# Kernel optimization log

Hardware: AMD Instinct MI355X
Metric: run time of the kernel (lower is better)

## Reference

```python
import jax, jax.numpy as jnp
import numpy as np

B, S, D, H, HD = 2, 1024, 1024, 16, 64
CKV, CQ, R, DFF, L, V = 256, 384, 32, 2816, 4, 32000
EPS = 1.1920929e-07  # torch RMSNorm default eps = finfo(float32).eps


def rmsnorm(x, w):
    return x * jax.lax.rsqrt(jnp.mean(x * x, -1, keepdims=True) + EPS) * w


def rope(x, base=10000.0):
    # x: [B, H, S, d]; GPT-NeoX style rotate-half, matches RoPE._neg_half
    d, s = x.shape[-1], x.shape[2]
    theta = 1.0 / base ** (jnp.arange(0, d, 2, dtype=jnp.float32) / d)
    ang = jnp.arange(s, dtype=jnp.float32)[:, None] * theta[None, :]
    ang = jnp.concatenate([ang, ang], -1)  # [s, d]
    neg = jnp.concatenate([-x[..., d // 2:], x[..., :d // 2]], -1)
    return x * jnp.cos(ang) + neg * jnp.sin(ang)


def forward(tokens, embed, w_kv_down, b_kv_down, w_q_down, b_q_down, w_kv_up, b_kv_up,
            w_q_up, b_q_up, w_o, b_o, kv_norm_w, q_norm_w, norm1_w, norm2_w,
            w_in, b_in, w_out, b_out, norm_f_w, w_head, b_head):
    h = embed[tokens]                                  # [B, S, D]
    causal = jnp.triu(jnp.ones((S, S), bool), 1)       # True above diagonal -> masked
    scale = np.float32(1.0 / np.sqrt(HD + R))
    for i in range(L):
        xn = rmsnorm(h, norm1_w[i])
        ckv = xn @ w_kv_down[i] + b_kv_down[i]         # [B, S, CKV+R]
        c_kv, k_rope = ckv[..., :CKV], ckv[..., CKV:]
        kv = rmsnorm(c_kv, kv_norm_w[i]) @ w_kv_up[i] + b_kv_up[i]
        kv = kv.reshape(B, S, H, 2 * HD).transpose(0, 2, 1, 3)  # [B, H, S, 2*HD]
        k, v = kv[..., :HD], kv[..., HD:]
        qf = rmsnorm(xn @ w_q_down[i] + b_q_down[i], q_norm_w[i]) @ w_q_up[i] + b_q_up[i]
        qf = qf.reshape(B, S, H, HD + R).transpose(0, 2, 1, 3)   # [B, H, S, HD+R]
        q, q_rope = qf[..., :HD], qf[..., HD:]
        k_rope = rope(k_rope[:, None, :, :])           # [B, 1, S, R], shared across heads
        q_rope = rope(q_rope)
        k = jnp.concatenate([k, jnp.broadcast_to(k_rope, (B, H, S, R))], -1)
        q = jnp.concatenate([q, q_rope], -1)
        a = jnp.einsum('bhqd,bhkd->bhqk', q, k) * scale
        a = jax.nn.softmax(jnp.where(causal, -jnp.inf, a), -1)
        attn = jnp.einsum('bhqk,bhkd->bhqd', a, v).transpose(0, 2, 1, 3).reshape(B, S, D)
        h = h + attn @ w_o[i] + b_o[i]
        uv = rmsnorm(h, norm2_w[i]) @ w_in[i] + b_in[i]  # [B, S, 2*DFF]
        h = h + (uv[..., :DFF] * jax.nn.silu(uv[..., DFF:])) @ w_out[i] + b_out[i]
    return rmsnorm(h, norm_f_w) @ w_head + b_head        # [B, S, V]


def setup_inputs() -> dict:
    key = jax.random.key(0)
    it = iter(jax.random.split(key, 24))
    w = lambda shp: jax.random.normal(next(it), shp, jnp.float32) * 0.02
    return dict(
        tokens=jax.random.randint(next(it), (B, S), 0, V),
        embed=w((V, D)),
        w_kv_down=w((L, D, CKV + R)), b_kv_down=w((L, CKV + R)),
        w_q_down=w((L, D, CQ)), b_q_down=w((L, CQ)),
        w_kv_up=w((L, CKV, 2 * HD * H)), b_kv_up=w((L, 2 * HD * H)),
        w_q_up=w((L, CQ, (HD + R) * H)), b_q_up=w((L, (HD + R) * H)),
        w_o=w((L, D, D)), b_o=w((L, D)),
        kv_norm_w=jnp.ones((L, CKV)), q_norm_w=jnp.ones((L, CQ)),
        norm1_w=jnp.ones((L, D)), norm2_w=jnp.ones((L, D)),
        w_in=w((L, D, 2 * DFF)), b_in=w((L, 2 * DFF)),
        w_out=w((L, DFF, D)), b_out=w((L, D)),
        norm_f_w=jnp.ones((D,)),
        w_head=w((D, V)), b_head=w((V,)),
    )


def reference(tokens, embed, w_kv_down, b_kv_down, w_q_down, b_q_down, w_kv_up, b_kv_up,
              w_q_up, b_q_up, w_o, b_o, kv_norm_w, q_norm_w, norm1_w, norm2_w,
              w_in, b_in, w_out, b_out, norm_f_w, w_head, b_head):
    return forward(tokens, embed, w_kv_down, b_kv_down, w_q_down, b_q_down, w_kv_up,
                   b_kv_up, w_q_up, b_q_up, w_o, b_o, kv_norm_w, q_norm_w, norm1_w,
                   norm2_w, w_in, b_in, w_out, b_out, norm_f_w, w_head, b_head)
```

## Files before the change

kernel.cpp:

```cpp
#include <hip/hip_runtime.h>
#include <cstdint>
#include <cstddef>

typedef unsigned short u16;
typedef __attribute__((__ext_vector_type__(8))) __bf16 bf16x8;
typedef __attribute__((__ext_vector_type__(4))) float f32x4;
typedef __attribute__((__ext_vector_type__(8))) unsigned short u16x8;

#define DEVI __device__ __forceinline__

constexpr int Bb = 2, Ss = 1024, Dd = 1024, Hh = 16;
constexpr int Mm = Bb * Ss;
constexpr int QKD = 128;
constexpr float EPSF = 1.1920929e-07f;
constexpr float NEG = -1e30f;
constexpr float QSCALE = 0.10206207261596577f;
constexpr float LOG1E4_16 = 9.210340371976184f / 16.f;

DEVI u16 f2b(float f) {
  union { float f; uint32_t u; } a; a.f = f;
  uint32_t r = a.u + 0x7FFFu + ((a.u >> 16) & 1u);
  return (u16)(r >> 16);
}
DEVI float b2f(u16 h) {
  union { uint32_t u; float f; } a; a.u = ((uint32_t)h) << 16; return a.f;
}

struct WJob { const float* src; u16* dst; int K; int N; int perm; int ntiles; };
struct WJobs { WJob j[7]; };

__global__ __launch_bounds__(256) void k_wcvt_batch(WJobs jobs, int njobs) {
  int t = blockIdx.x;
  int ji = 0;
  while (ji < njobs - 1 && t >= jobs.j[ji].ntiles) { t -= jobs.j[ji].ntiles; ++ji; }
  const float* __restrict__ src = jobs.j[ji].src;
  u16* __restrict__ dst = jobs.j[ji].dst;
  const int K = jobs.j[ji].K, N = jobs.j[ji].N, perm = jobs.j[ji].perm;
  const int ktiles = K >> 6;
  const int bk = (t % ktiles) * 64;
  const int bn = (t / ktiles) * 64;
  __shared__ float ts[64][65];
  const int tid = threadIdx.x;
  {
    int c4 = tid & 15, r = tid >> 4;
    #pragma unroll
    for (int p = 0; p < 4; ++p) {
      int row = r + p * 16;
      int col = bn + c4 * 4;
      float4 v = make_float4(0.f, 0.f, 0.f, 0.f);
      if (col < N) v = *(const float4*)(src + (size_t)(bk + row) * N + col);
      ts[row][c4 * 4 + 0] = v.x; ts[row][c4 * 4 + 1] = v.y;
      ts[row][c4 * 4 + 2] = v.z; ts[row][c4 * 4 + 3] = v.w;
    }
  }
  __syncthreads();
  {
    int k8 = tid & 7, c = tid >> 3;
    #pragma unroll
    for (int p = 0; p < 2; ++p) {
      int cc = c + p * 32;
      int gcol = bn + cc;
      int row = perm ? ((gcol < 2816) ? (gcol * 2) : ((gcol - 2816) * 2 + 1)) : gcol;
      u16x8 o;
      #pragma unroll
      for (int q = 0; q < 8; ++q) o[q] = f2b(ts[k8 * 8 + q][cc]);
      *(u16x8*)(dst + (size_t)row * K + bk + k8 * 8) = o;
    }
  }
}

__global__ void k_embed(const int* __restrict__ tok, const float* __restrict__ emb,
                        float* __restrict__ h) {
  int m = blockIdx.x;
  int t = tok[m];
  const float4* src = (const float4*)(emb + (size_t)t * Dd);
  float4* dst = (float4*)(h + (size_t)m * Dd);
  dst[threadIdx.x] = src[threadIdx.x];
}

__global__ void k_rms(const float* __restrict__ in, int inStride,
                      const float* __restrict__ w, u16* __restrict__ out, int K) {
  int m = blockIdx.x;
  const float* x = in + (size_t)m * inStride;
  float ss = 0.f;
  for (int i = threadIdx.x; i < K; i += 256) { float v = x[i]; ss += v * v; }
  #pragma unroll
  for (int off = 32; off; off >>= 1) ss += __shfl_xor(ss, off);
  __shared__ float red[4];
  if ((threadIdx.x & 63) == 0) red[threadIdx.x >> 6] = ss;
  __syncthreads();
  float r = rsqrtf((red[0] + red[1] + red[2] + red[3]) / (float)K + EPSF);
  for (int i = threadIdx.x; i < K; i += 256)
    out[(size_t)m * K + i] = f2b(x[i] * r * w[i]);
}

__global__ void k_biascat(const float* __restrict__ b1, const float* __restrict__ b2,
                          float* __restrict__ out) {
  int i = blockIdx.x * 256 + threadIdx.x;
  float v = 0.f;
  if (i < 288) v = b1[i];
  else if (i >= 384) v = b2[i - 384];
  out[i] = v;
}

__global__ void k_buildqk(const float* __restrict__ qf, const u16* __restrict__ kv,
                          const float* __restrict__ ckvq, u16* __restrict__ Q,
                          u16* __restrict__ Kb) {
  int s = blockIdx.x, bh = blockIdx.y;
  int b = bh >> 4, h = bh & 15;
  int d = threadIdx.x;
  int m = b * Ss + s;
  int j = d - 64;
  float sn = 0.f, cs = 0.f;
  if (d >= 64 && d < 96) {
    float theta = __expf(-(float)(j & 15) * LOG1E4_16);
    __sincosf((float)s * theta, &sn, &cs);
  }
  const float* qrow = qf + (size_t)m * (Hh * 96) + h * 96;
  float qv = 0.f;
  if (d < 64) qv = qrow[d];
  else if (d < 96) {
    float x = qrow[64 + j], o = qrow[64 + (j ^ 16)];
    qv = x * cs + ((j < 16) ? -o : o) * sn;
  }
  Q[((size_t)bh * Ss + s) * QKD + d] = f2b(qv * QSCALE);
  u16 kvv = 0;
  if (d < 64) kvv = kv[(size_t)m * 2048 + h * 128 + d];
  else if (d < 96) {
    const float* rr = ckvq + (size_t)m * 768 + 256;
    float x = rr[j], o = rr[j ^ 16];
    kvv = f2b(x * cs + ((j < 16) ? -o : o) * sn);
  }
  Kb[((size_t)bh * Ss + s) * QKD + d] = kvv;
}

__global__ void k_buildvt(const u16* __restrict__ kv, u16* __restrict__ Vt) {
  __shared__ u16 t[32][33];
  int bh = blockIdx.x, s0 = blockIdx.y * 32, d0 = blockIdx.z * 32;
  int b = bh >> 4, h = bh & 15;
  int tx = threadIdx.x, ty = threadIdx.y;
  #pragma unroll
  for (int i = ty; i < 32; i += 8) {
    int s = s0 + i, d = d0 + tx;
    t[i][tx] = kv[(size_t)(b * Ss + s) * 2048 + h * 128 + 64 + d];
  }
  __syncthreads();
  #pragma unroll
  for (int i = ty; i < 32; i += 8) {
    int d = d0 + i, s = s0 + tx;
    Vt[((size_t)bh * 64 + d) * Ss + s] = t[tx][i];
  }
}

#define GAS __attribute__((address_space(1)))
#define LAS __attribute__((address_space(3)))
DEVI void gll16(const void* g, void* l) {
  __builtin_amdgcn_global_load_lds((GAS const void*)g, (LAS void*)l, 16, 0, 0);
}
#define VMW(n) asm volatile("s_waitcnt vmcnt(" #n ")" ::: "memory")
#define FENCE asm volatile("" ::: "memory")

__global__ __launch_bounds__(256) void k_flash(
    const u16* __restrict__ Qg, const u16* __restrict__ Kg,
    const u16* __restrict__ Vtg, u16* __restrict__ attn) {
  __shared__ u16 lK[2][64 * 128];
  __shared__ u16 lV[2][64 * 64];
  __shared__ u16 lP[4][16 * 64];
  const int tid = threadIdx.x;
  const int qt = blockIdx.x, bh = blockIdx.y;
  const int b = bh >> 4, h = bh & 15;
  const int lane = tid & 63, w = tid >> 6;
  const int g = lane >> 4, fr = lane & 15;
  const u16* Qh = Qg + (size_t)bh * Ss * QKD;
  const u16* Kh = Kg + (size_t)bh * Ss * QKD;
  const u16* Vh = Vtg + (size_t)bh * 64 * Ss;

  auto stageKV = [&](int buf, int kt) {
    int r = tid >> 4, c = tid & 15;
    #pragma unroll
    for (int gg = 0; gg < 4; ++gg) {
      int row = gg * 16 + r;
      const u16* src = Kh + (size_t)(kt * 64 + row) * QKD + ((c ^ (row & 7)) * 8);
      gll16(src, (u16*)lK[buf] + gg * 2048 + tid * 8);
    }
    int r2 = tid >> 3, c2 = tid & 7;
    #pragma unroll
    for (int gg = 0; gg < 2; ++gg) {
      int d = gg * 32 + r2;
      const u16* src = Vh + (size_t)d * Ss + kt * 64 + ((c2 ^ (d & 7)) * 8);
      gll16(src, (u16*)lV[buf] + gg * 2048 + tid * 8);
    }
  };

  const int q0 = qt * 64;
  bf16x8 af[4];
  const u16* qrow = Qh + (size_t)(q0 + w * 16 + fr) * QKD + g * 8;
  #pragma unroll
  for (int k4 = 0; k4 < 4; ++k4) af[k4] = *(const bf16x8*)(qrow + k4 * 32);

  f32x4 acc_o[4] = {};
  float mrow = NEG, lrow = 0.f;

  stageKV(0, 0);

  for (int kt = 0; kt <= qt; ++kt) {
    const int cur = kt & 1;
    if (kt < qt) { stageKV(cur ^ 1, kt + 1); VMW(6); }
    else { VMW(0); }
    __builtin_amdgcn_s_barrier();
    FENCE;

    f32x4 accs[4] = {};
    #pragma unroll
    for (int j = 0; j < 4; ++j) {
      #pragma unroll
      for (int k4 = 0; k4 < 4; ++k4) {
        int row = j * 16 + fr;
        int ch = (k4 * 4 + g) ^ (row & 7);
        bf16x8 kf = *(const bf16x8*)&lK[cur][row * 128 + ch * 8];
        accs[j] = __builtin_amdgcn_mfma_f32_16x16x32_bf16(kf, af[k4], accs[j], 0, 0, 0);
      }
    }

    float p[16];
    float tmax = NEG;
    #pragma unroll
    for (int j = 0; j < 4; ++j)
      #pragma unroll
      for (int r = 0; r < 4; ++r) {
        float s = accs[j][r];
        int kloc = j * 16 + 4 * g + r;
        bool valid = (kt < qt) || (kloc <= w * 16 + fr);
        s = valid ? s : NEG;
        p[j * 4 + r] = s;
        tmax = fmaxf(tmax, s);
      }
    tmax = fmaxf(tmax, __shfl_xor(tmax, 16));
    tmax = fmaxf(tmax, __shfl_xor(tmax, 32));
    float mnew = fmaxf(mrow, tmax);
    float scale = __expf(mrow - mnew);
    float tsum = 0.f;
    #pragma unroll
    for (int i = 0; i < 16; ++i) { p[i] = __expf(p[i] - mnew); tsum += p[i]; }
    tsum += __shfl_xor(tsum, 16);
    tsum += __shfl_xor(tsum, 32);
    lrow = lrow * scale + tsum;
    mrow = mnew;

    #pragma unroll
    for (int j = 0; j < 4; ++j)
      #pragma unroll
      for (int t = 0; t < 2; ++t) {
        uint32_t u = (uint32_t)f2b(p[j * 4 + 2 * t]) |
                     ((uint32_t)f2b(p[j * 4 + 2 * t + 1]) << 16);
        int kp = 8 * j + 2 * g + t;
        int ch = kp >> 2, wi = kp & 3;
        ((uint32_t*)lP[w])[fr * 32 + ((ch ^ (fr & 7)) << 2) + wi] = u;
      }

    float sc_q[4];
    #pragma unroll
    for (int r = 0; r < 4; ++r) sc_q[r] = __shfl(scale, 4 * g + r);
    #pragma unroll
    for (int j2 = 0; j2 < 4; ++j2)
      #pragma unroll
      for (int r = 0; r < 4; ++r) acc_o[j2][r] *= sc_q[r];

    #pragma unroll
    for (int ksub = 0; ksub < 2; ++ksub) {
      int chp = (4 * ksub + g) ^ (fr & 7);
      bf16x8 pa = *(const bf16x8*)&((const u16*)lP[w])[fr * 64 + chp * 8];
      #pragma unroll
      for (int j2 = 0; j2 < 4; ++j2) {
        int d = j2 * 16 + fr;
        int chv = (ksub * 4 + g) ^ (d & 7);
        bf16x8 vf = *(const bf16x8*)&lV[cur][d * 64 + chv * 8];
        acc_o[j2] = __builtin_amdgcn_mfma_f32_16x16x32_bf16(pa, vf, acc_o[j2], 0, 0, 0);
      }
    }
    FENCE;
    __builtin_amdgcn_s_barrier();
    FENCE;
  }

  float li[4];
  #pragma unroll
  for (int r = 0; r < 4; ++r) li[r] = 1.f / __shfl(lrow, 4 * g + r);
  #pragma unroll
  for (int j2 = 0; j2 < 4; ++j2)
    #pragma unroll
    for (int r = 0; r < 4; ++r) {
      int q = q0 + w * 16 + 4 * g + r;
      int d = j2 * 16 + fr;
      attn[((size_t)(b * Ss) + q) * Dd + h * 64 + d] = f2b(acc_o[j2][r] * li[r]);
    }
}

template <int MODE>
__global__ __launch_bounds__(512, 4) void k_gemm256b(
    const u16* __restrict__ A, const u16* __restrict__ Bt,
    const float* __restrict__ bias, void* __restrict__ Cv,
    int N, int K) {
  __shared__ u16 lA[2][128 * 32];
  __shared__ u16 lB[2][256 * 32];
  const int tid = threadIdx.x;
  const int gx = gridDim.x;
  const int nwg = gx * gridDim.y;
  const int f = blockIdx.y * gx + blockIdx.x;
  const int f2 = (f & 7) * (nwg >> 3) + (f >> 3);
  const int bx = f2 % gx, by = f2 / gx;
  const long m0 = (long)bx * 128, n0 = (long)by * 256;
  const int lane = tid & 63, wid = tid >> 6;
  const int wm = (wid >> 2) * 64, wn = (wid & 3) * 64;
  const int fr = lane & 15, l4 = lane >> 4;
  const int sw = (fr >> 1) & 3;

  const int ra = tid >> 2;
  const int ca = ((tid & 3) ^ ((ra >> 1) & 3)) * 8;
  const u16* a0 = A + (m0 + ra) * (long)K + ca;
  const int rb = tid >> 2;
  const int cb0 = ((tid & 3) ^ ((rb >> 1) & 3)) * 8;
  const int cb1 = ((tid & 3) ^ (((rb + 128) >> 1) & 3)) * 8;
  const u16* b0 = Bt + (n0 + rb) * (long)K + cb0;
  const u16* b1 = Bt + (n0 + rb + 128) * (long)K + cb1;

  f32x4 acc[4][4] = {};
  const int NT = K >> 5;

  gll16(a0, (u16*)lA[0] + tid * 8);
  gll16(b0, (u16*)lB[0] + tid * 8);
  gll16(b1, (u16*)lB[0] + 4096 + tid * 8);

  for (int j = 0; j < NT; ++j) {
    const int cur = j & 1;
    const int kk1 = (j + 1) << 5;
    if (j + 1 < NT) {
      gll16(a0 + kk1, (u16*)lA[cur ^ 1] + tid * 8);
      gll16(b0 + kk1, (u16*)lB[cur ^ 1] + tid * 8);
      gll16(b1 + kk1, (u16*)lB[cur ^ 1] + 4096 + tid * 8);
      VMW(3);
    } else {
      VMW(0);
    }
    __builtin_amdgcn_s_barrier();
    FENCE;
    bf16x8 af[4], bfv[4];
    #pragma unroll
    for (int i = 0; i < 4; ++i)
      af[i] = *(const bf16x8*)&lA[cur][(wm + i * 16 + fr) * 32 + ((l4 ^ sw) * 8)];
    #pragma unroll
    for (int jj = 0; jj < 4; ++jj)
      bfv[jj] = *(const bf16x8*)&lB[cur][(wn + jj * 16 + fr) * 32 + ((l4 ^ sw) * 8)];
    #pragma unroll
    for (int i = 0; i < 4; ++i)
      #pragma unroll
      for (int jj = 0; jj < 4; ++jj)
        acc[i][jj] = __builtin_amdgcn_mfma_f32_16x16x32_bf16(af[i], bfv[jj], acc[i][jj], 0, 0, 0);
    FENCE;
    __builtin_amdgcn_s_barrier();
    FENCE;
  }

  const long r0 = m0 + wm + l4 * 4;
  const long c0 = n0 + wn + fr;
  if (MODE == 0) {
    float* C = (float*)Cv;
    #pragma unroll
    for (int j = 0; j < 4; ++j) {
      long col = c0 + j * 16;
      float bs = bias[col];
      #pragma unroll
      for (int i = 0; i < 4; ++i)
        #pragma unroll
        for (int r = 0; r < 4; ++r)
          C[(r0 + i * 16 + r) * (long)N + col] = acc[i][j][r] + bs;
    }
  } else {
    u16* G = (u16*)Cv;
    #pragma unroll
    for (int j = 0; j < 4; ++j) {
      long col = c0 + j * 16;
      int pcol = (int)((col & 1) ? (col >> 1) + 2816 : (col >> 1));
      float bs = bias[pcol];
      #pragma unroll
      for (int i = 0; i < 4; ++i)
        #pragma unroll
        for (int r = 0; r < 4; ++r) {
          float val = acc[i][j][r] + bs;
          float oth = __shfl_xor(val, 1);
          if (!(col & 1)) {
            float x = oth;
            float gv = val * x * (1.f / (1.f + __expf(-x)));
            G[(r0 + i * 16 + r) * 2816L + (col >> 1)] = f2b(gv);
          }
        }
    }
  }
}

template <int MODE, int BN, bool SWZ>
__global__ __launch_bounds__(256, 4) void k_gemm(
    const u16* __restrict__ A, const u16* __restrict__ Bt,
    const float* __restrict__ bias, void* __restrict__ C,
    int N, int K, long sA, long sB, long sC) {
  __shared__ u16 lA[2][128 * 32];
  __shared__ u16 lB[2][BN * 32];
  const int tid = threadIdx.x;
  const int bz = blockIdx.z;

  int bx, by;
  if (SWZ) {
    int gx = gridDim.x;
    int nwg = gx * gridDim.y;
    int f = blockIdx.y * gx + blockIdx.x;
    int f2 = (f & 7) * (nwg >> 3) + (f >> 3);
    bx = f2 % gx; by = f2 / gx;
  } else {
    bx = blockIdx.x; by = blockIdx.y;
  }
  const long m0 = (long)bx * 128, n0 = (long)by * BN;

  const u16* Az = A + (size_t)bz * sA;
  const u16* Bz = Bt + (size_t)bz * sB;
  const int srow = tid >> 2;
  const int scol = (tid & 3) << 3;
  const u16* a0 = Az + (m0 + srow) * (long)K + scol;
  const u16* b0 = Bz + (n0 + srow) * (long)K + scol;
  const long rstep = 64L * K;

  const int lane = tid & 63, wid = tid >> 6;
  constexpr int WR = (BN == 128) ? 64 : 32;
  constexpr int MI = WR / 16;
  const int wm = (BN == 128) ? (wid >> 1) * 64 : wid * 32;
  const int wn = (BN == 128) ? (wid & 1) * 64 : 0;
  const int fr = lane & 15, kg = (lane >> 4) * 8;

  f32x4 acc[MI][4] = {};
  const int NT = K >> 5;

  gll16(a0, (u16*)lA[0] + tid * 8);
  gll16(a0 + rstep, (u16*)lA[0] + 2048 + tid * 8);
  gll16(b0, (u16*)lB[0] + tid * 8);
  if (BN == 128) gll16(b0 + rstep, (u16*)lB[0] + 2048 + tid * 8);

  for (int j = 0; j < NT; ++j) {
    const int cur = j & 1;
    const int kk1 = (j + 1) << 5;
    if (j + 1 < NT) {
      gll16(a0 + kk1, (u16*)lA[cur ^ 1] + tid * 8);
      gll16(a0 + rstep + kk1, (u16*)lA[cur ^ 1] + 2048 + tid * 8);
      gll16(b0 + kk1, (u16*)lB[cur ^ 1] + tid * 8);
      if (BN == 128) {
        gll16(b0 + rstep + kk1, (u16*)lB[cur ^ 1] + 2048 + tid * 8);
        VMW(4);
      } else {
        VMW(3);
      }
    } else {
      VMW(0);
    }
    __builtin_amdgcn_s_barrier();
    FENCE;
    bf16x8 af[MI], bfr[4];
    #pragma unroll
    for (int i = 0; i < MI; i++) af[i] = *(const bf16x8*)&lA[cur][(wm + i * 16 + fr) * 32 + kg];
    #pragma unroll
    for (int jj = 0; jj < 4; jj++) bfr[jj] = *(const bf16x8*)&lB[cur][(wn + jj * 16 + fr) * 32 + kg];
    #pragma unroll
    for (int i = 0; i < MI; i++)
      #pragma unroll
      for (int jj = 0; jj < 4; jj++)
        acc[i][jj] = __builtin_amdgcn_mfma_f32_16x16x32_bf16(af[i], bfr[jj], acc[i][jj], 0, 0, 0);
    FENCE;
    __builtin_amdgcn_s_barrier();
    FENCE;
  }

  const int rb = wm + ((lane >> 4) << 2);
  const int cb = wn + (lane & 15);
  #pragma unroll
  for (int j = 0; j < 4; j++) {
    long gcol = n0 + cb + j * 16;
    float bs = 0.f;
    if (gcol < N) bs = bias[gcol];
    #pragma unroll
    for (int i = 0; i < MI; i++) {
      #pragma unroll
      for (int r = 0; r < 4; r++) {
        long grow = m0 + rb + i * 16 + r;
        float val = acc[i][j][r];
        if (gcol < N) {
          if (MODE == 0) {
            ((float*)C)[grow * N + gcol] = val + bs;
          } else if (MODE == 1) {
            float* p = (float*)C + grow * N + gcol; *p += val + bs;
          } else {
            ((u16*)C)[grow * N + gcol] = f2b(val + bs);
          }
        }
      }
    }
  }
}

extern "C" void kernel_launch(void* const* d_in, const int* in_sizes, int n_in,
                              void* d_out, int out_size, void* d_ws, size_t ws_size,
                              hipStream_t stream) {
  (void)in_sizes; (void)n_in; (void)out_size; (void)ws_size;
  const int*   tokens    = (const int*)  d_in[0];
  const float* embed     = (const float*)d_in[1];
  const float* w_kv_down = (const float*)d_in[2];
  const float* b_kv_down = (const float*)d_in[3];
  const float* w_q_down  = (const float*)d_in[4];
  const float* b_q_down  = (const float*)d_in[5];
  const float* w_kv_up   = (const float*)d_in[6];
  const float* b_kv_up   = (const float*)d_in[7];
  const float* w_q_up    = (const float*)d_in[8];
  const float* b_q_up    = (const float*)d_in[9];
  const float* w_o       = (const float*)d_in[10];
  const float* b_o       = (const float*)d_in[11];
  const float* kv_norm_w = (const float*)d_in[12];
  const float* q_norm_w  = (const float*)d_in[13];
  const float* norm1_w   = (const float*)d_in[14];
  const float* norm2_w   = (const float*)d_in[15];
  const float* w_in      = (const float*)d_in[16];
  const float* b_in      = (const float*)d_in[17];
  const float* w_out     = (const float*)d_in[18];
  const float* b_out     = (const float*)d_in[19];
  const float* norm_f_w  = (const float*)d_in[20];
  const float* w_head    = (const float*)d_in[21];
  const float* b_head    = (const float*)d_in[22];

  char* base = (char*)d_ws;
  size_t off = 0;
  auto alloc = [&](size_t bytes) -> void* {
    void* p = base + off;
    off += (bytes + 255) & ~(size_t)255;
    return p;
  };
  u16* warena = (u16*)alloc((size_t)32000 * 1024 * 2);
  u16* wT_dq    = warena;
  u16* wT_kvup  = wT_dq   + 768 * 1024;
  u16* wT_qup   = wT_kvup + 2048 * 256;
  u16* wT_o     = wT_qup  + 1536 * 384;
  u16* wT_in    = wT_o    + 1024 * 1024;
  u16* wT_out   = wT_in   + 5632 * 1024;

  float* h     = (float*)alloc((size_t)Mm * 1024 * 4);
  u16*   xn    = (u16*)  alloc((size_t)Mm * 1024 * 2);
  float* ckvq  = (float*)alloc((size_t)Mm * 768 * 4);
  float* bdq   = (float*)alloc(768 * 4);
  u16*   ckvn  = (u16*)  alloc((size_t)Mm * 256 * 2);
  u16*   kv    = (u16*)  alloc((size_t)Mm * 2048 * 2);
  u16*   qdn   = (u16*)  alloc((size_t)Mm * 384 * 2);
  float* qf    = (float*)alloc((size_t)Mm * 1536 * 4);
  u16*   Qb    = (u16*)  alloc((size_t)32 * 1024 * QKD * 2);
  u16*   Kb    = (u16*)  alloc((size_t)32 * 1024 * QKD * 2);
  u16*   Vt    = (u16*)  alloc((size_t)32 * 64 * 1024 * 2);
  u16*   attn  = (u16*)  alloc((size_t)Mm * 1024 * 2);
  u16*   gate  = (u16*)  alloc((size_t)Mm * 2816 * 2);

  dim3 tb(32, 8);

  k_embed<<<Mm, 256, 0, stream>>>(tokens, embed, h);

  for (int l = 0; l < 4; l++) {
    WJobs jb;
    jb.j[0] = { w_kv_down + (size_t)l * 1024 * 288,  wT_dq,              1024, 288,  0, 96 };
    jb.j[1] = { w_q_down  + (size_t)l * 1024 * 384,  wT_dq + 384 * 1024, 1024, 384,  0, 96 };
    jb.j[2] = { w_kv_up   + (size_t)l * 256 * 2048,  wT_kvup,            256,  2048, 0, 128 };
    jb.j[3] = { w_q_up    + (size_t)l * 384 * 1536,  wT_qup,             384,  1536, 0, 144 };
    jb.j[4] = { w_o       + (size_t)l * 1024 * 1024, wT_o,               1024, 1024, 0, 256 };
    jb.j[5] = { w_in      + (size_t)l * 1024 * 5632, wT_in,              1024, 5632, 1, 1408 };
    jb.j[6] = { w_out     + (size_t)l * 2816 * 1024, wT_out,             2816, 1024, 0, 704 };
    k_wcvt_batch<<<2832, 256, 0, stream>>>(jb, 7);
    k_biascat<<<3, 256, 0, stream>>>(b_kv_down + l * 288, b_q_down + l * 384, bdq);

    k_rms<<<Mm, 256, 0, stream>>>(h, 1024, norm1_w + l * 1024, xn, 1024);
    k_gemm<0, 64, true><<<dim3(16, 12), 256, 0, stream>>>(xn, wT_dq, bdq,
                                                          ckvq, 768, 1024, 0, 0, 0);
    k_rms<<<Mm, 256, 0, stream>>>(ckvq, 768, kv_norm_w + l * 256, ckvn, 256);
    k_gemm<2, 128, true><<<dim3(16, 16), 256, 0, stream>>>(ckvn, wT_kvup, b_kv_up + l * 2048,
                                                           kv, 2048, 256, 0, 0, 0);
    k_rms<<<Mm, 256, 0, stream>>>(ckvq + 384, 768, q_norm_w + l * 384, qdn, 384);
    k_gemm<0, 128, true><<<dim3(16, 12), 256, 0, stream>>>(qdn, wT_qup, b_q_up + l * 1536,
                                                           qf, 1536, 384, 0, 0, 0);
    k_buildqk<<<dim3(Ss, 32), 128, 0, stream>>>(qf, kv, ckvq, Qb, Kb);
    k_buildvt<<<dim3(32, 32, 2), tb, 0, stream>>>(kv, Vt);
    k_flash<<<dim3(16, 32), 256, 0, stream>>>(Qb, Kb, Vt, attn);
    k_gemm<1, 64, true><<<dim3(16, 16), 256, 0, stream>>>(attn, wT_o, b_o + l * 1024,
                                                          h, 1024, 1024, 0, 0, 0);
    k_rms<<<Mm, 256, 0, stream>>>(h, 1024, norm2_w + l * 1024, xn, 1024);
    k_gemm256b<1><<<dim3(16, 22), 512, 0, stream>>>(xn, wT_in, b_in + l * 5632,
                                                    gate, 5632, 1024);
    k_gemm<1, 64, true><<<dim3(16, 16), 256, 0, stream>>>(gate, wT_out, b_out + l * 1024,
                                                          h, 1024, 2816, 0, 0, 0);
  }

  k_rms<<<Mm, 256, 0, stream>>>(h, 1024, norm_f_w, xn, 1024);
  {
    WJobs jbh;
    jbh.j[0] = { w_head, warena, 1024, 32000, 0, 8000 };
    k_wcvt_batch<<<8000, 256, 0, stream>>>(jbh, 1);
  }
  k_gemm256b<0><<<dim3(16, 125), 512, 0, stream>>>(xn, warena, b_head,
                                                   (float*)d_out, 32000, 1024);
}
```

Measured before the change: 1.184 ms.

## Generalize GEMM tiling to BMxBN with swizzled LDS and smaller tiles for layer GEMMs

Replaces the per-layer k_gemm with a template parameterized by BM and BN, using a 2x2 wave layout and an XOR-swizzled LDS layout to reduce bank conflicts. The down/up projections, output projection and FFN-out GEMMs now use 64x64 or 64x128 tiles, which doubles the workgroup count and improves CU occupancy for these small-N problems. The FFN-in GEMM with the fused SwiGLU moves from the 512-thread 128x256 kernel to a 256-thread 128x128 variant. Smaller tiles give more parallelism in exchange for more global traffic per FLOP.

```diff
diff --git a/kernel.cpp b/kernel.cpp
--- a/kernel.cpp
+++ b/kernel.cpp
@@ -296,10 +296,9 @@
     }
 }
 
-template <int MODE>
 __global__ __launch_bounds__(512, 4) void k_gemm256b(
     const u16* __restrict__ A, const u16* __restrict__ Bt,
-    const float* __restrict__ bias, void* __restrict__ Cv,
+    const float* __restrict__ bias, float* __restrict__ C,
     int N, int K) {
   __shared__ u16 lA[2][128 * 32];
   __shared__ u16 lB[2][256 * 32];
@@ -363,27 +362,100 @@
 
   const long r0 = m0 + wm + l4 * 4;
   const long c0 = n0 + wn + fr;
-  if (MODE == 0) {
-    float* C = (float*)Cv;
-    #pragma unroll
-    for (int j = 0; j < 4; ++j) {
-      long col = c0 + j * 16;
-      float bs = bias[col];
-      #pragma unroll
-      for (int i = 0; i < 4; ++i)
-        #pragma unroll
-        for (int r = 0; r < 4; ++r)
-          C[(r0 + i * 16 + r) * (long)N + col] = acc[i][j][r] + bs;
-    }
-  } else {
-    u16* G = (u16*)Cv;
-    #pragma unroll
-    for (int j = 0; j < 4; ++j) {
+  #pragma unroll
+  for (int j = 0; j < 4; ++j) {
+    long col = c0 + j * 16;
+    float bs = bias[col];
+    #pragma unroll
+    for (int i = 0; i < 4; ++i)
+      #pragma unroll
+      for (int r = 0; r < 4; ++r)
+        C[(r0 + i * 16 + r) * (long)N + col] = acc[i][j][r] + bs;
+  }
+}
+
+template <int MODE, int BM, int BN>
+__global__ __launch_bounds__(256, 4) void k_gemm(
+    const u16* __restrict__ A, const u16* __restrict__ Bt,
+    const float* __restrict__ bias, void* __restrict__ C,
+    int N, int K) {
+  constexpr int MI = BM / 32, NJ = BN / 32;
+  constexpr int AL = BM / 64, BL = BN / 64;
+  __shared__ u16 lA[2][BM * 32];
+  __shared__ u16 lB[2][BN * 32];
+  const int tid = threadIdx.x;
+  const int gx = gridDim.x;
+  const int nwg = gx * gridDim.y;
+  const int f = blockIdx.y * gx + blockIdx.x;
+  const int f2 = (f & 7) * (nwg >> 3) + (f >> 3);
+  const int bx = f2 % gx, by = f2 / gx;
+  const long m0 = (long)bx * BM, n0 = (long)by * BN;
+  const int lane = tid & 63, wid = tid >> 6;
+  const int wm = (wid >> 1) * (BM / 2), wn = (wid & 1) * (BN / 2);
+  const int fr = lane & 15, l4 = lane >> 4;
+  const int sw = (fr >> 1) & 3;
+
+  const int rs = tid >> 2;
+  const int cs = ((tid & 3) ^ ((rs >> 1) & 3)) * 8;
+  const u16* a0 = A + (m0 + rs) * (long)K + cs;
+  const u16* b0 = Bt + (n0 + rs) * (long)K + cs;
+  const long g64 = 64L * K;
+
+  f32x4 acc[MI][NJ] = {};
+  const int NT = K >> 5;
+
+  auto stage = [&](int buf, int kk) {
+    #pragma unroll
+    for (int g = 0; g < AL; ++g)
+      gll16(a0 + g * g64 + kk, (u16*)lA[buf] + g * 2048 + tid * 8);
+    #pragma unroll
+    for (int g = 0; g < BL; ++g)
+      gll16(b0 + g * g64 + kk, (u16*)lB[buf] + g * 2048 + tid * 8);
+  };
+
+  stage(0, 0);
+
+  for (int j = 0; j < NT; ++j) {
+    const int cur = j & 1;
+    const int kk1 = (j + 1) << 5;
+    if (j + 1 < NT) {
+      stage(cur ^ 1, kk1);
+      if constexpr (AL + BL == 2) VMW(2);
+      else if constexpr (AL + BL == 3) VMW(3);
+      else VMW(4);
+    } else {
+      VMW(0);
+    }
+    __builtin_amdgcn_s_barrier();
+    FENCE;
+    bf16x8 af[MI], bfr[NJ];
+    #pragma unroll
+    for (int i = 0; i < MI; i++)
+      af[i] = *(const bf16x8*)&lA[cur][(wm + i * 16 + fr) * 32 + ((l4 ^ sw) * 8)];
+    #pragma unroll
+    for (int jj = 0; jj < NJ; jj++)
+      bfr[jj] = *(const bf16x8*)&lB[cur][(wn + jj * 16 + fr) * 32 + ((l4 ^ sw) * 8)];
+    #pragma unroll
+    for (int i = 0; i < MI; i++)
+      #pragma unroll
+      for (int jj = 0; jj < NJ; jj++)
+        acc[i][jj] = __builtin_amdgcn_mfma_f32_16x16x32_bf16(af[i], bfr[jj], acc[i][jj], 0, 0, 0);
+    FENCE;
+    __builtin_amdgcn_s_barrier();
+    FENCE;
+  }
+
+  const long r0 = m0 + wm + l4 * 4;
+  const long c0 = n0 + wn + fr;
+  if (MODE == 3) {
+    u16* G = (u16*)C;
+    #pragma unroll
+    for (int j = 0; j < NJ; ++j) {
       long col = c0 + j * 16;
       int pcol = (int)((col & 1) ? (col >> 1) + 2816 : (col >> 1));
       float bs = bias[pcol];
       #pragma unroll
-      for (int i = 0; i < 4; ++i)
+      for (int i = 0; i < MI; ++i)
         #pragma unroll
         for (int r = 0; r < 4; ++r) {
           float val = acc[i][j][r] + bs;
@@ -395,110 +467,21 @@
           }
         }
     }
-  }
-}
-
-template <int MODE, int BN, bool SWZ>
-__global__ __launch_bounds__(256, 4) void k_gemm(
-    const u16* __restrict__ A, const u16* __restrict__ Bt,
-    const float* __restrict__ bias, void* __restrict__ C,
-    int N, int K, long sA, long sB, long sC) {
-  __shared__ u16 lA[2][128 * 32];
-  __shared__ u16 lB[2][BN * 32];
-  const int tid = threadIdx.x;
-  const int bz = blockIdx.z;
-
-  int bx, by;
-  if (SWZ) {
-    int gx = gridDim.x;
-    int nwg = gx * gridDim.y;
-    int f = blockIdx.y * gx + blockIdx.x;
-    int f2 = (f & 7) * (nwg >> 3) + (f >> 3);
-    bx = f2 % gx; by = f2 / gx;
   } else {
-    bx = blockIdx.x; by = blockIdx.y;
-  }
-  const long m0 = (long)bx * 128, n0 = (long)by * BN;
-
-  const u16* Az = A + (size_t)bz * sA;
-  const u16* Bz = Bt + (size_t)bz * sB;
-  const int srow = tid >> 2;
-  const int scol = (tid & 3) << 3;
-  const u16* a0 = Az + (m0 + srow) * (long)K + scol;
-  const u16* b0 = Bz + (n0 + srow) * (long)K + scol;
-  const long rstep = 64L * K;
-
-  const int lane = tid & 63, wid = tid >> 6;
-  constexpr int WR = (BN == 128) ? 64 : 32;
-  constexpr int MI = WR / 16;
-  const int wm = (BN == 128) ? (wid >> 1) * 64 : wid * 32;
-  const int wn = (BN == 128) ? (wid & 1) * 64 : 0;
-  const int fr = lane & 15, kg = (lane >> 4) * 8;
-
-  f32x4 acc[MI][4] = {};
-  const int NT = K >> 5;
-
-  gll16(a0, (u16*)lA[0] + tid * 8);
-  gll16(a0 + rstep, (u16*)lA[0] + 2048 + tid * 8);
-  gll16(b0, (u16*)lB[0] + tid * 8);
-  if (BN == 128) gll16(b0 + rstep, (u16*)lB[0] + 2048 + tid * 8);
-
-  for (int j = 0; j < NT; ++j) {
-    const int cur = j & 1;
-    const int kk1 = (j + 1) << 5;
-    if (j + 1 < NT) {
-      gll16(a0 + kk1, (u16*)lA[cur ^ 1] + tid * 8);
-      gll16(a0 + rstep + kk1, (u16*)lA[cur ^ 1] + 2048 + tid * 8);
-      gll16(b0 + kk1, (u16*)lB[cur ^ 1] + tid * 8);
-      if (BN == 128) {
-        gll16(b0 + rstep + kk1, (u16*)lB[cur ^ 1] + 2048 + tid * 8);
-        VMW(4);
-      } else {
-        VMW(3);
-      }
-    } else {
-      VMW(0);
-    }
-    __builtin_amdgcn_s_barrier();
-    FENCE;
-    bf16x8 af[MI], bfr[4];
-    #pragma unroll
-    for (int i = 0; i < MI; i++) af[i] = *(const bf16x8*)&lA[cur][(wm + i * 16 + fr) * 32 + kg];
-    #pragma unroll
-    for (int jj = 0; jj < 4; jj++) bfr[jj] = *(const bf16x8*)&lB[cur][(wn + jj * 16 + fr) * 32 + kg];
-    #pragma unroll
-    for (int i = 0; i < MI; i++)
-      #pragma unroll
-      for (int jj = 0; jj < 4; jj++)
-        acc[i][jj] = __builtin_amdgcn_mfma_f32_16x16x32_bf16(af[i], bfr[jj], acc[i][jj], 0, 0, 0);
-    FENCE;
-    __builtin_amdgcn_s_barrier();
-    FENCE;
-  }
-
-  const int rb = wm + ((lane >> 4) << 2);
-  const int cb = wn + (lane & 15);
-  #pragma unroll
-  for (int j = 0; j < 4; j++) {
-    long gcol = n0 + cb + j * 16;
-    float bs = 0.f;
-    if (gcol < N) bs = bias[gcol];
-    #pragma unroll
-    for (int i = 0; i < MI; i++) {
-      #pragma unroll
-      for (int r = 0; r < 4; r++) {
-        long grow = m0 + rb + i * 16 + r;
-        float val = acc[i][j][r];
-        if (gcol < N) {
-          if (MODE == 0) {
-            ((float*)C)[grow * N + gcol] = val + bs;
-          } else if (MODE == 1) {
-            float* p = (float*)C + grow * N + gcol; *p += val + bs;
-          } else {
-            ((u16*)C)[grow * N + gcol] = f2b(val + bs);
-          }
+    #pragma unroll
+    for (int j = 0; j < NJ; ++j) {
+      long col = c0 + j * 16;
+      float bs = bias[col];
+      #pragma unroll
+      for (int i = 0; i < MI; ++i)
+        #pragma unroll
+        for (int r = 0; r < 4; ++r) {
+          long row = r0 + i * 16 + r;
+          float val = acc[i][j][r] + bs;
+          if (MODE == 0) ((float*)C)[row * N + col] = val;
+          else if (MODE == 1) { float* p = (float*)C + row * N + col; *p += val; }
+          else ((u16*)C)[row * N + col] = f2b(val);
         }
-      }
     }
   }
 }
@@ -577,24 +560,23 @@
     k_biascat<<<3, 256, 0, stream>>>(b_kv_down + l * 288, b_q_down + l * 384, bdq);
 
     k_rms<<<Mm, 256, 0, stream>>>(h, 1024, norm1_w + l * 1024, xn, 1024);
-    k_gemm<0, 64, true><<<dim3(16, 12), 256, 0, stream>>>(xn, wT_dq, bdq,
-                                                          ckvq, 768, 1024, 0, 0, 0);
+    k_gemm<0, 64, 64><<<dim3(32, 12), 256, 0, stream>>>(xn, wT_dq, bdq, ckvq, 768, 1024);
     k_rms<<<Mm, 256, 0, stream>>>(ckvq, 768, kv_norm_w + l * 256, ckvn, 256);
-    k_gemm<2, 128, true><<<dim3(16, 16), 256, 0, stream>>>(ckvn, wT_kvup, b_kv_up + l * 2048,
-                                                           kv, 2048, 256, 0, 0, 0);
+    k_gemm<2, 64, 128><<<dim3(32, 16), 256, 0, stream>>>(ckvn, wT_kvup, b_kv_up + l * 2048,
+                                                         kv, 2048, 256);
     k_rms<<<Mm, 256, 0, stream>>>(ckvq + 384, 768, q_norm_w + l * 384, qdn, 384);
-    k_gemm<0, 128, true><<<dim3(16, 12), 256, 0, stream>>>(qdn, wT_qup, b_q_up + l * 1536,
-                                                           qf, 1536, 384, 0, 0, 0);
+    k_gemm<0, 64, 64><<<dim3(32, 24), 256, 0, stream>>>(qdn, wT_qup, b_q_up + l * 1536,
+                                                        qf, 1536, 384);
     k_buildqk<<<dim3(Ss, 32), 128, 0, stream>>>(qf, kv, ckvq, Qb, Kb);
     k_buildvt<<<dim3(32, 32, 2), tb, 0, stream>>>(kv, Vt);
     k_flash<<<dim3(16, 32), 256, 0, stream>>>(Qb, Kb, Vt, attn);
-    k_gemm<1, 64, true><<<dim3(16, 16), 256, 0, stream>>>(attn, wT_o, b_o + l * 1024,
-                                                          h, 1024, 1024, 0, 0, 0);
+    k_gemm<1, 64, 64><<<dim3(32, 16), 256, 0, stream>>>(attn, wT_o, b_o + l * 1024,
+                                                        h, 1024, 1024);
     k_rms<<<Mm, 256, 0, stream>>>(h, 1024, norm2_w + l * 1024, xn, 1024);
-    k_gemm256b<1><<<dim3(16, 22), 512, 0, stream>>>(xn, wT_in, b_in + l * 5632,
-                                                    gate, 5632, 1024);
-    k_gemm<1, 64, true><<<dim3(16, 16), 256, 0, stream>>>(gate, wT_out, b_out + l * 1024,
-                                                          h, 1024, 2816, 0, 0, 0);
+    k_gemm<3, 128, 128><<<dim3(16, 44), 256, 0, stream>>>(xn, wT_in, b_in + l * 5632,
+                                                          gate, 5632, 1024);
+    k_gemm<1, 64, 64><<<dim3(32, 16), 256, 0, stream>>>(gate, wT_out, b_out + l * 1024,
+                                                        h, 1024, 2816);
   }
 
   k_rms<<<Mm, 256, 0, stream>>>(h, 1024, norm_f_w, xn, 1024);
@@ -603,6 +585,6 @@
     jbh.j[0] = { w_head, warena, 1024, 32000, 0, 8000 };
     k_wcvt_batch<<<8000, 256, 0, stream>>>(jbh, 1);
   }
-  k_gemm256b<0><<<dim3(16, 125), 512, 0, stream>>>(xn, warena, b_head,
-                                                   (float*)d_out, 32000, 1024);
-}
+  k_gemm256b<<<dim3(16, 125), 512, 0, stream>>>(xn, warena, b_head,
+                                                (float*)d_out, 32000, 1024);
+}
```

New measurement: 1.070 ms. 9.6% less time.
